# Kernel optimization log

Hardware: AMD Instinct MI355X
Metric: run time of the kernel (lower is better)

Reference implementation:

```python
import jax, jax.numpy as jnp
import numpy as np

NB, NLOC, NALL, NNEI, A_SEL = 1, 512, 640, 96, 20
N_DIM, E_DIM, A_DIM, AXIS = 128, 64, 64, 4
EDGE_INFO = 2 * N_DIM + E_DIM          # 320
SYM = AXIS * (E_DIM + N_DIM)           # 768, cal_1_dim
ANGLE = A_DIM + N_DIM + 2 * E_DIM      # 320, angle_dim


def setup_inputs() -> dict:
    key = jax.random.key(0)
    ks = jax.random.split(key, 16)
    nrm = lambda k, sh, s=1.0: jax.random.normal(k, sh, dtype=jnp.float32) * s

    def lin(k, din, dout, s=0.05):
        k1, k2 = jax.random.split(k)
        return nrm(k1, (din, dout), s), nrm(k2, (dout,), s)

    inp = {}
    inp["g1_ext"] = nrm(ks[0], (NB, NALL, N_DIM))
    inp["g2"] = nrm(ks[1], (NB, NLOC, NNEI, E_DIM))
    inp["h2"] = nrm(ks[2], (NB, NLOC, NNEI, 3))
    inp["angle_embed"] = nrm(ks[3], (NB, NLOC, A_SEL, A_SEL, A_DIM))
    inp["sw"] = jax.random.uniform(ks[4], (NB, NLOC, NNEI), dtype=jnp.float32)
    inp["a_sw"] = jax.random.uniform(ks[5], (NB, NLOC, A_SEL), dtype=jnp.float32)
    inp["w_self"], inp["b_self"] = lin(ks[6], N_DIM, N_DIM)
    inp["w_proj"] = nrm(ks[7], (E_DIM, N_DIM), 0.05)  # proj_g1g2, bias=False
    inp["w_lin1"], inp["b_lin1"] = lin(ks[8], SYM, N_DIM)
    inp["w_edge1"], inp["b_edge1"] = lin(ks[9], EDGE_INFO, N_DIM)
    inp["w_lin2"], inp["b_lin2"] = lin(ks[10], EDGE_INFO, E_DIM)
    inp["w_ang"], inp["b_ang"] = lin(ks[11], ANGLE, A_DIM)
    inp["w_ga1"], inp["b_ga1"] = lin(ks[12], ANGLE, E_DIM)
    inp["w_ga2"], inp["b_ga2"] = lin(ks[13], E_DIM, E_DIM)
    inp["nlist"] = jax.random.randint(ks[14], (NB, NLOC, NNEI), 0, NALL)
    inp["nlist_mask"] = jnp.ones((NB, NLOC, NNEI), dtype=bool)
    inp["a_nlist_mask"] = jnp.ones((NB, NLOC, A_SEL), dtype=bool)
    return inp


def _sym_op(g, h2, mask, sw, axis):
    # symmetrization_op: _cal_hg (smooth, use_sqrt_nnei) followed by _cal_grrg
    # g: nb x nloc x nnei x d, h2: nb x nloc x nnei x 3
    g = jnp.where(mask[..., None], g, 0.0) * sw[..., None]
    inv = np.float32(1.0 / np.sqrt(g.shape[2]))
    hg = jnp.einsum('blnt,blnd->bltd', h2, g) * inv
    grrg = jnp.einsum('bltd,blta->blda', hg, hg[..., :axis])  # nb x nloc x d x axis
    return grrg.reshape(grrg.shape[0], grrg.shape[1], -1)


def reference(g1_ext, g2, h2, angle_embed, sw, a_sw,
              w_self, b_self, w_proj, w_lin1, b_lin1, w_edge1, b_edge1,
              w_lin2, b_lin2, w_ang, b_ang, w_ga1, b_ga1, w_ga2, b_ga2,
              nlist, nlist_mask, a_nlist_mask):
    act = jax.nn.silu
    nb, nloc, nnei, e_dim = g2.shape
    n_dim = g1_ext.shape[-1]
    a_sel = angle_embed.shape[2]
    g1 = g1_ext[:, :nloc]
    # _make_nei_g1: gather neighbor node features, nb x nloc x nnei x n_dim
    gg1 = jnp.take_along_axis(
        g1_ext, nlist.reshape(nb, nloc * nnei, 1), axis=1
    ).reshape(nb, nloc, nnei, n_dim)
    maskf = nlist_mask[..., None]
    swf = sw[..., None]

    g1_update = [g1]
    # node self mlp
    g1_update.append(act(g1 @ w_self + b_self))
    # conv update: masked+switched gg1 times projected g2, mean over nnei
    gg1_ms = jnp.where(maskf, gg1, 0.0) * swf
    g1_update.append(jnp.sum((g2 @ w_proj) * gg1_ms, axis=2) / np.float32(nnei))
    # symmetrized axis-neuron update
    sym = jnp.concatenate(
        [_sym_op(g2, h2, nlist_mask, sw, AXIS),
         _sym_op(gg1, h2, nlist_mask, sw, AXIS)], axis=-1)
    g1_update.append(act(sym @ w_lin1 + b_lin1))
    # edge info: [tiled g1, gg1, g2] -> 2*n_dim + e_dim
    edge_info = jnp.concatenate(
        [jnp.broadcast_to(g1[:, :, None, :], (nb, nloc, nnei, n_dim)), gg1, g2],
        axis=-1)
    g1_edge = act(edge_info @ w_edge1 + b_edge1) * swf
    g1_update.append(jnp.sum(g1_edge, axis=2) / np.float32(nnei))
    # res_avg
    g1_new = sum(g1_update) / np.float32(np.sqrt(len(g1_update)))

    g2_update = [g2, act(edge_info @ w_lin2 + b_lin2)]

    # angle branch: angle_dim = a_dim + n_dim + 2*e_dim
    g2a = jnp.where(a_nlist_mask[..., None], g2[:, :, :a_sel, :], 0.0)
    ang = jnp.concatenate([
        angle_embed,
        jnp.broadcast_to(g1[:, :, None, None, :], (nb, nloc, a_sel, a_sel, n_dim)),
        jnp.broadcast_to(g2a[:, :, :, None, :], (nb, nloc, a_sel, a_sel, e_dim)),
        jnp.broadcast_to(g2a[:, :, None, :, :], (nb, nloc, a_sel, a_sel, e_dim)),
    ], axis=-1)
    a_new = (angle_embed + act(ang @ w_ang + b_ang)) / np.float32(np.sqrt(2.0))

    # angle -> edge message, switch-weighted on both angle axes, mean over one axis
    ang_w = ang * a_sw[:, :, :, None, None] * a_sw[:, :, None, :, None]
    g2_ang = jnp.sum(act(ang_w @ w_ga1 + b_ga1), axis=3) / np.float32(a_sel)
    g2_ang_full = jnp.concatenate(
        [g2_ang, jnp.zeros((nb, nloc, nnei - a_sel, e_dim), g2.dtype)], axis=2)
    g2_update.append(act(g2_ang_full @ w_ga2 + b_ga2))
    g2_new = sum(g2_update) / np.float32(np.sqrt(len(g2_update)))

    return g1_new, g2_new, h2, a_new
```

## Files before the change

kernel.cpp:

```cpp
#include <hip/hip_runtime.h>
#include <hip/hip_bf16.h>

#define NLOC 512
#define NALL 640
#define NNEI 96
#define ASEL 20
#define NDIM 128
#define EDIM 64
#define ADIM 64

typedef short bf16x8 __attribute__((ext_vector_type(8)));
typedef float f32x4 __attribute__((ext_vector_type(4)));
typedef unsigned short ushort8 __attribute__((ext_vector_type(8)));

__device__ __forceinline__ unsigned short f2bf(float f) {
    unsigned int u = __float_as_uint(f);
    unsigned int r = (u + 0x7FFFu + ((u >> 16) & 1u)) >> 16;
    return (unsigned short)r;
}
__device__ __forceinline__ float bf2f(unsigned short u) {
    return __uint_as_float(((unsigned int)u) << 16);
}
__device__ __forceinline__ float silu(float x) { return x / (1.0f + __expf(-x)); }

__device__ __forceinline__ void cvt8_store(unsigned short* dst, const float* src) {
    float4 f0 = *(const float4*)src;
    float4 f1 = *(const float4*)(src + 4);
    ushort8 v;
    v[0] = f2bf(f0.x); v[1] = f2bf(f0.y); v[2] = f2bf(f0.z); v[3] = f2bf(f0.w);
    v[4] = f2bf(f1.x); v[5] = f2bf(f1.y); v[6] = f2bf(f1.z); v[7] = f2bf(f1.w);
    *(ushort8*)dst = v;
}

__global__ void prep_bt2(const float* __restrict__ w_ang, const float* __restrict__ w_ga1,
                         const float* __restrict__ w_edge1, const float* __restrict__ w_lin2,
                         const float* __restrict__ w_proj, const float* __restrict__ w_self,
                         unsigned short* __restrict__ bt_ae, unsigned short* __restrict__ bt_g2e,
                         unsigned short* __restrict__ bt_sm, unsigned short* __restrict__ bt_pij) {
    int idx = blockIdx.x * 256 + threadIdx.x;
    if (idx < 8192) {
        int k = idx & 63, n = idx >> 6;
        bt_ae[idx] = f2bf((n < 64) ? w_ang[k * 64 + n] : w_ga1[k * 64 + (n - 64)]);
    } else if (idx < 32768) {
        int id2 = idx - 8192;
        int k = id2 & 63, n = id2 >> 6;
        float v;
        if (n < 128)      v = w_edge1[(256 + k) * 128 + n];
        else if (n < 192) v = w_lin2[(256 + k) * 64 + (n - 128)];
        else if (n < 256) v = 0.0f;
        else              v = w_proj[k * 128 + (n - 256)];
        bt_g2e[id2] = f2bf(v);
    } else if (idx < 114688) {
        int id3 = idx - 32768;
        int k = id3 & 127, n = id3 >> 7;
        float v;
        if (n < 128)      v = w_edge1[k * 128 + n];
        else if (n < 192) v = w_lin2[k * 64 + (n - 128)];
        else if (n < 320) v = w_edge1[(128 + k) * 128 + (n - 192)];
        else if (n < 384) v = w_lin2[(128 + k) * 64 + (n - 320)];
        else if (n < 512) { int c = n - 384;
            v = (c < 64) ? w_ang[(64 + k) * 64 + c] : w_ga1[(64 + k) * 64 + (c - 64)]; }
        else              v = w_self[k * 128 + (n - 512)];
        bt_sm[id3] = f2bf(v);
    } else {
        int id4 = idx - 114688;
        int k = id4 & 63, n = id4 >> 6;
        float v;
        if (n < 128) v = (n < 64) ? w_ang[(192 + k) * 64 + n] : w_ga1[(192 + k) * 64 + (n - 64)];
        else { int c = n - 128;
            v = (c < 64) ? w_ang[(256 + k) * 64 + c] : w_ga1[(256 + k) * 64 + (c - 64)]; }
        bt_pij[id4] = f2bf(v);
    }
}

__global__ __launch_bounds__(256) void gemm_small(
    const float* __restrict__ g1_ext, const unsigned short* __restrict__ bt_sm,
    const float* __restrict__ b_self, float* __restrict__ P1a, float* __restrict__ g1self,
    float* __restrict__ E1, float* __restrict__ E2) {
    const int m0 = blockIdx.x * 128;
    const int ntile = blockIdx.y;
    __shared__ __align__(16) unsigned short Asl[128 * 136];
    __shared__ __align__(16) unsigned short Bsl[128 * 136];
    const int tid = threadIdx.x;
#pragma unroll
    for (int u = 0; u < 8; u++) {
        int g = tid + u * 256;
        int row = g >> 4, seg = g & 15;
        cvt8_store(&Asl[row * 136 + seg * 8], g1_ext + (m0 + row) * 128 + seg * 8);
        *(ushort8*)&Bsl[row * 136 + seg * 8] =
            *(const ushort8*)&bt_sm[(ntile * 128 + row) * 128 + seg * 8];
    }
    __syncthreads();
    const int lane = tid & 63, wid = tid >> 6;
    const int wr = wid >> 1, wc = wid & 1;
    const int r15 = lane & 15, kg = lane >> 4;
    f32x4 acc[4][4] = {};
#pragma unroll
    for (int h = 0; h < 4; h++) {
        bf16x8 afr[4], bfr[4];
#pragma unroll
        for (int mi = 0; mi < 4; mi++)
            afr[mi] = *(const bf16x8*)&Asl[(wr * 64 + mi * 16 + r15) * 136 + h * 32 + kg * 8];
#pragma unroll
        for (int ni = 0; ni < 4; ni++)
            bfr[ni] = *(const bf16x8*)&Bsl[(wc * 64 + ni * 16 + r15) * 136 + h * 32 + kg * 8];
#pragma unroll
        for (int mi = 0; mi < 4; mi++)
#pragma unroll
            for (int ni = 0; ni < 4; ni++)
                acc[mi][ni] = __builtin_amdgcn_mfma_f32_16x16x32_bf16(afr[mi], bfr[ni], acc[mi][ni], 0, 0, 0);
    }
#pragma unroll
    for (int mi = 0; mi < 4; mi++) {
        int rbase = m0 + wr * 64 + mi * 16 + kg * 4;
#pragma unroll
        for (int ni = 0; ni < 4; ni++) {
            int gc = ntile * 128 + wc * 64 + ni * 16 + r15;
#pragma unroll
            for (int t2 = 0; t2 < 4; t2++) {
                int a = rbase + t2;
                float z = acc[mi][ni][t2];
                if (gc < 192) { if (a < 512) E1[a * 192 + gc] = z; }
                else if (gc < 384) E2[a * 192 + (gc - 192)] = z;
                else if (gc < 512) { if (a < 512) P1a[a * 128 + (gc - 384)] = z; }
                else { if (a < 512) g1self[a * 128 + (gc - 512)] = silu(z + b_self[gc - 512]); }
            }
        }
    }
}

__global__ __launch_bounds__(256) void gemm_pij(
    const float* __restrict__ g2, const unsigned short* __restrict__ bt_pij,
    unsigned short* __restrict__ P_i, unsigned short* __restrict__ P_j) {
    const int m0 = blockIdx.x * 128;
    const int ntile = blockIdx.y;
    __shared__ __align__(16) unsigned short Asl[128 * 72];
    __shared__ __align__(16) unsigned short Bsl[128 * 72];
    const int tid = threadIdx.x;
#pragma unroll
    for (int u = 0; u < 4; u++) {
        int g = tid + u * 256;
        int row = g >> 3, seg = g & 7;
        int li = m0 + row, l = li / 20, i = li - l * 20;
        cvt8_store(&Asl[row * 72 + seg * 8], g2 + (l * 96 + i) * 64 + seg * 8);
        *(ushort8*)&Bsl[row * 72 + seg * 8] =
            *(const ushort8*)&bt_pij[(ntile * 128 + row) * 64 + seg * 8];
    }
    __syncthreads();
    const int lane = tid & 63, wid = tid >> 6;
    const int wr = wid >> 1, wc = wid & 1;
    const int r15 = lane & 15, kg = lane >> 4;
    f32x4 acc[4][4] = {};
#pragma unroll
    for (int h = 0; h < 2; h++) {
        bf16x8 afr[4], bfr[4];
#pragma unroll
        for (int mi = 0; mi < 4; mi++)
            afr[mi] = *(const bf16x8*)&Asl[(wr * 64 + mi * 16 + r15) * 72 + h * 32 + kg * 8];
#pragma unroll
        for (int ni = 0; ni < 4; ni++)
            bfr[ni] = *(const bf16x8*)&Bsl[(wc * 64 + ni * 16 + r15) * 72 + h * 32 + kg * 8];
#pragma unroll
        for (int mi = 0; mi < 4; mi++)
#pragma unroll
            for (int ni = 0; ni < 4; ni++)
                acc[mi][ni] = __builtin_amdgcn_mfma_f32_16x16x32_bf16(afr[mi], bfr[ni], acc[mi][ni], 0, 0, 0);
    }
    unsigned short* Pout = (ntile == 0) ? P_i : P_j;
#pragma unroll
    for (int mi = 0; mi < 4; mi++) {
        int rbase = m0 + wr * 64 + mi * 16 + kg * 4;
#pragma unroll
        for (int ni = 0; ni < 4; ni++) {
            int c = wc * 64 + ni * 16 + r15;
#pragma unroll
            for (int t2 = 0; t2 < 4; t2++)
                Pout[(rbase + t2) * 128 + c] = f2bf(acc[mi][ni][t2]);
        }
    }
}

__global__ void k_sym(const float* __restrict__ g1_ext, const float* __restrict__ g2,
                      const float* __restrict__ h2, const float* __restrict__ sw,
                      const int* __restrict__ nlist, const float* __restrict__ w_lin1,
                      const float* __restrict__ b_lin1, float* __restrict__ term4) {
    int l = blockIdx.x, t = threadIdx.x;
    __shared__ float h2s[96 * 3];
    __shared__ float sws[96];
    __shared__ int nls[96];
    __shared__ float hg[3 * 192];
    __shared__ float symv[768];
    if (t < 96) { sws[t] = sw[l * 96 + t]; nls[t] = nlist[l * 96 + t]; }
    for (int p = t; p < 288; p += 256) h2s[p] = h2[l * 288 + p];
    __syncthreads();
    const float inv = 0.1020620726f;
    for (int p = t; p < 576; p += 256) {
        float acc = 0.0f;
        if (p < 192) {
            int tt = p >> 6, d = p & 63;
            for (int n = 0; n < 96; n++)
                acc += h2s[n * 3 + tt] * g2[(l * 96 + n) * 64 + d] * sws[n];
            hg[tt * 192 + d] = acc * inv;
        } else {
            int q = p - 192;
            int tt = q >> 7, d = q & 127;
            for (int n = 0; n < 96; n++)
                acc += h2s[n * 3 + tt] * g1_ext[nls[n] * 128 + d] * sws[n];
            hg[tt * 192 + 64 + d] = acc * inv;
        }
    }
    __syncthreads();
    for (int p = t; p < 768; p += 256) {
        float acc = 0.0f;
        if (p < 256) {
            int d = p >> 2, a = p & 3;
            for (int tt = 0; tt < 3; tt++) acc += hg[tt * 192 + d] * hg[tt * 192 + a];
        } else {
            int q = p - 256;
            int d = q >> 2, a = q & 3;
            for (int tt = 0; tt < 3; tt++) acc += hg[tt * 192 + 64 + d] * hg[tt * 192 + 64 + a];
        }
        symv[p] = acc;
    }
    __syncthreads();
    if (t < 128) {
        float acc = b_lin1[t];
#pragma unroll 8
        for (int k = 0; k < 768; k++) acc += symv[k] * w_lin1[k * 128 + t];
        term4[l * 128 + t] = silu(acc);
    }
}

__global__ __launch_bounds__(256) void angle_main(
    const float* __restrict__ ae, const unsigned short* __restrict__ bt_ae,
    const float* __restrict__ P1a, const unsigned short* __restrict__ P_i,
    const unsigned short* __restrict__ P_j, const float* __restrict__ a_sw,
    const float* __restrict__ b_ang, const float* __restrict__ b_ga1,
    float* __restrict__ g2acc, float* __restrict__ a_new_out) {
    const int m0 = blockIdx.x * 128;
    __shared__ __align__(16) unsigned short Asl[128 * 72];
    __shared__ __align__(16) unsigned short Bsl[128 * 72];
    const int tid = threadIdx.x;
#pragma unroll
    for (int u = 0; u < 4; u++) {
        int g = tid + u * 256;
        int row = g >> 3, seg = g & 7;
        cvt8_store(&Asl[row * 72 + seg * 8], ae + (m0 + row) * 64 + seg * 8);
        *(ushort8*)&Bsl[row * 72 + seg * 8] = *(const ushort8*)&bt_ae[row * 64 + seg * 8];
    }
    __syncthreads();
    const int lane = tid & 63, wid = tid >> 6;
    const int wr = wid >> 1, wc = wid & 1;
    const int r15 = lane & 15, kg = lane >> 4;
    f32x4 acc[4][4] = {};
#pragma unroll
    for (int h = 0; h < 2; h++) {
        bf16x8 afr[4], bfr[4];
#pragma unroll
        for (int mi = 0; mi < 4; mi++)
            afr[mi] = *(const bf16x8*)&Asl[(wr * 64 + mi * 16 + r15) * 72 + h * 32 + kg * 8];
#pragma unroll
        for (int ni = 0; ni < 4; ni++)
            bfr[ni] = *(const bf16x8*)&Bsl[(wc * 64 + ni * 16 + r15) * 72 + h * 32 + kg * 8];
#pragma unroll
        for (int mi = 0; mi < 4; mi++)
#pragma unroll
            for (int ni = 0; ni < 4; ni++)
                acc[mi][ni] = __builtin_amdgcn_mfma_f32_16x16x32_bf16(afr[mi], bfr[ni], acc[mi][ni], 0, 0, 0);
    }
#pragma unroll
    for (int mi = 0; mi < 4; mi++) {
        int rbase = m0 + wr * 64 + mi * 16 + kg * 4;
        int l = rbase / 400;
        int rem = rbase - l * 400;
        int i = rem / 20;
        int j0 = rem - i * 20;
        const float* p1b = P1a + l * 128;
        const unsigned short* pib = P_i + (l * 20 + i) * 128;
        const unsigned short* pjb = P_j + l * 20 * 128;
#pragma unroll
        for (int ni = 0; ni < 4; ni++) {
            int c = wc * 64 + ni * 16 + r15;
            float base = p1b[c] + bf2f(pib[c]);
            if (c < 64) {
                float bb = b_ang[c];
#pragma unroll
                for (int t2 = 0; t2 < 4; t2++) {
                    int r = rbase + t2, j = j0 + t2;
                    float z = acc[mi][ni][t2] + base + bf2f(pjb[j * 128 + c]);
                    float aev = bf2f(Asl[(rbase - m0 + t2) * 72 + c]);
                    a_new_out[r * 64 + c] = (aev + silu(z + bb)) * 0.70710678f;
                }
            } else {
                int cc = c - 64;
                float bb = b_ga1[cc];
                float swi = a_sw[l * 20 + i];
                float part = 0.0f;
#pragma unroll
                for (int t2 = 0; t2 < 4; t2++) {
                    int j = j0 + t2;
                    float z = acc[mi][ni][t2] + base + bf2f(pjb[j * 128 + c]);
                    float s = swi * a_sw[l * 20 + j];
                    part += silu(s * z + bb);
                }
                atomicAdd(&g2acc[(l * 20 + i) * 64 + cc], part);
            }
        }
    }
}

__global__ void k_f2(const float* __restrict__ g2ang_acc, const float* __restrict__ w_ga2,
                     const float* __restrict__ b_ga2, float* __restrict__ yga2) {
    int l = blockIdx.x, t = threadIdx.x;
    __shared__ float gs[20 * 64];
    for (int p = t; p < 1280; p += 256) gs[p] = g2ang_acc[l * 1280 + p] * 0.05f;
    __syncthreads();
    for (int p = t; p < 1280; p += 256) {
        int i = p >> 6, c = p & 63;
        float acc = b_ga2[c];
#pragma unroll 8
        for (int k = 0; k < 64; k++) acc += gs[i * 64 + k] * w_ga2[k * 64 + c];
        yga2[l * 1280 + p] = silu(acc);
    }
}

__global__ __launch_bounds__(256) void edge_main(
    const float* __restrict__ g1_ext, const float* __restrict__ g2, const float* __restrict__ sw,
    const int* __restrict__ nlist, const unsigned short* __restrict__ bt_g2e,
    const float* __restrict__ E1, const float* __restrict__ E2,
    const float* __restrict__ b_edge1, const float* __restrict__ b_lin2,
    const float* __restrict__ b_ga2, const float* __restrict__ yga2,
    float* __restrict__ g1_acc3, float* __restrict__ g1_acc5, float* __restrict__ g2_new_out) {
    const int m0 = blockIdx.x * 128;
    const int ntile = blockIdx.y;
    __shared__ __align__(16) unsigned short Asl[128 * 72];
    __shared__ __align__(16) unsigned short Bsl[128 * 72];
    const int tid = threadIdx.x;
#pragma unroll
    for (int u = 0; u < 4; u++) {
        int g = tid + u * 256;
        int row = g >> 3, seg = g & 7;
        cvt8_store(&Asl[row * 72 + seg * 8], g2 + (m0 + row) * 64 + seg * 8);
        *(ushort8*)&Bsl[row * 72 + seg * 8] =
            *(const ushort8*)&bt_g2e[(ntile * 128 + row) * 64 + seg * 8];
    }
    __syncthreads();
    const int lane = tid & 63, wid = tid >> 6;
    const int wr = wid >> 1, wc = wid & 1;
    const int r15 = lane & 15, kg = lane >> 4;
    f32x4 acc[4][4] = {};
#pragma unroll
    for (int h = 0; h < 2; h++) {
        bf16x8 afr[4], bfr[4];
#pragma unroll
        for (int mi = 0; mi < 4; mi++)
            afr[mi] = *(const bf16x8*)&Asl[(wr * 64 + mi * 16 + r15) * 72 + h * 32 + kg * 8];
#pragma unroll
        for (int ni = 0; ni < 4; ni++)
            bfr[ni] = *(const bf16x8*)&Bsl[(wc * 64 + ni * 16 + r15) * 72 + h * 32 + kg * 8];
#pragma unroll
        for (int mi = 0; mi < 4; mi++)
#pragma unroll
            for (int ni = 0; ni < 4; ni++)
                acc[mi][ni] = __builtin_amdgcn_mfma_f32_16x16x32_bf16(afr[mi], bfr[ni], acc[mi][ni], 0, 0, 0);
    }
#pragma unroll
    for (int mi = 0; mi < 4; mi++) {
        int rbase = m0 + wr * 64 + mi * 16 + kg * 4;
        int l = rbase / 96;
        int n0 = rbase - l * 96;
#pragma unroll
        for (int ni = 0; ni < 4; ni++) {
            int c = wc * 64 + ni * 16 + r15;
            if (ntile == 0) {
                float e1 = E1[l * 192 + c];
                float bb = b_edge1[c];
                float part = 0.0f;
#pragma unroll
                for (int t2 = 0; t2 < 4; t2++) {
                    int r = rbase + t2;
                    float z = acc[mi][ni][t2] + e1 + E2[nlist[r] * 192 + c];
                    part += silu(z + bb) * sw[r];
                }
                atomicAdd(&g1_acc5[l * 128 + c], part);
            } else if (ntile == 1) {
                if (c < 64) {
                    float e1 = E1[l * 192 + 128 + c];
                    float bb = b_lin2[c];
                    float sb = silu(b_ga2[c]);
#pragma unroll
                    for (int t2 = 0; t2 < 4; t2++) {
                        int r = rbase + t2, n = n0 + t2;
                        float z = acc[mi][ni][t2] + e1 + E2[nlist[r] * 192 + 128 + c];
                        float y = silu(z + bb);
                        float yg = (n < ASEL) ? yga2[(l * 20 + n) * 64 + c] : sb;
                        float g2v = bf2f(Asl[(r - m0) * 72 + c]);
                        g2_new_out[r * 64 + c] = (g2v + y + yg) * 0.57735027f;
                    }
                }
            } else {
                float part = 0.0f;
#pragma unroll
                for (int t2 = 0; t2 < 4; t2++) {
                    int r = rbase + t2;
                    part += acc[mi][ni][t2] * g1_ext[nlist[r] * 128 + c] * sw[r];
                }
                atomicAdd(&g1_acc3[l * 128 + c], part);
            }
        }
    }
}

__global__ void k_f1(const float* __restrict__ g1_ext, const float* __restrict__ g1self,
                     const float* __restrict__ acc3, const float* __restrict__ term4,
                     const float* __restrict__ acc5, float* __restrict__ out_g1) {
    int idx = blockIdx.x * 256 + threadIdx.x;
    float v = g1_ext[idx] + g1self[idx] + acc3[idx] * (1.0f / 96.0f) + term4[idx] +
              acc5[idx] * (1.0f / 96.0f);
    out_g1[idx] = v * 0.4472135955f;
}

extern "C" void kernel_launch(void* const* d_in, const int* in_sizes, int n_in,
                              void* d_out, int out_size, void* d_ws, size_t ws_size,
                              hipStream_t stream) {
    if (n_in < 22 || in_sizes[0] != 81920 || in_sizes[3] != 13107200) return;
    const float* g1_ext = (const float*)d_in[0];
    const float* g2     = (const float*)d_in[1];
    const float* h2     = (const float*)d_in[2];
    const float* ae     = (const float*)d_in[3];
    const float* sw     = (const float*)d_in[4];
    const float* a_sw   = (const float*)d_in[5];
    const float* w_self = (const float*)d_in[6];
    const float* b_self = (const float*)d_in[7];
    const float* w_proj = (const float*)d_in[8];
    const float* w_lin1 = (const float*)d_in[9];
    const float* b_lin1 = (const float*)d_in[10];
    const float* w_edge1= (const float*)d_in[11];
    const float* b_edge1= (const float*)d_in[12];
    const float* w_lin2 = (const float*)d_in[13];
    const float* b_lin2 = (const float*)d_in[14];
    const float* w_ang  = (const float*)d_in[15];
    const float* b_ang  = (const float*)d_in[16];
    const float* w_ga1  = (const float*)d_in[17];
    const float* b_ga1  = (const float*)d_in[18];
    const float* w_ga2  = (const float*)d_in[19];
    const float* b_ga2  = (const float*)d_in[20];
    const int*   nlist  = (const int*)d_in[21];

    float* ws = (float*)d_ws;
    unsigned short* bt_ae  = (unsigned short*)(ws);
    unsigned short* bt_g2e = (unsigned short*)(ws + 4096);
    unsigned short* bt_sm  = (unsigned short*)(ws + 16384);
    unsigned short* bt_pij = (unsigned short*)(ws + 57344);
    float* P1a    = ws + 65536;
    float* E1     = ws + 131072;
    float* E2     = ws + 229376;
    unsigned short* P_i = (unsigned short*)(ws + 352256);
    unsigned short* P_j = (unsigned short*)(ws + 1007616);
    float* g1self = ws + 1662976;
    float* term4  = ws + 1728512;
    float* yga2   = ws + 1794048;
    float* acc3   = ws + 2449408;
    float* acc5   = ws + 2514944;
    float* g2acc  = ws + 2580480;
    if (ws_size < (size_t)3235840 * sizeof(float)) return;

    float* out = (float*)d_out;
    float* out_g1 = out;
    float* out_g2 = out + 65536;
    float* out_h2 = out + 3211264;
    float* out_an = out + 3358720;

    hipMemsetAsync(acc3, 0, (65536 + 65536 + 655360) * sizeof(float), stream);

    prep_bt2<<<512, 256, 0, stream>>>(w_ang, w_ga1, w_edge1, w_lin2, w_proj, w_self,
                                      bt_ae, bt_g2e, bt_sm, bt_pij);
    gemm_small<<<dim3(5, 5), 256, 0, stream>>>(g1_ext, bt_sm, b_self, P1a, g1self, E1, E2);
    gemm_pij<<<dim3(80, 2), 256, 0, stream>>>(g2, bt_pij, P_i, P_j);
    k_sym<<<512, 256, 0, stream>>>(g1_ext, g2, h2, sw, nlist, w_lin1, b_lin1, term4);
    angle_main<<<1600, 256, 0, stream>>>(ae, bt_ae, P1a, P_i, P_j, a_sw, b_ang, b_ga1,
                                         g2acc, out_an);
    k_f2<<<512, 256, 0, stream>>>(g2acc, w_ga2, b_ga2, yga2);
    edge_main<<<dim3(384, 3), 256, 0, stream>>>(g1_ext, g2, sw, nlist, bt_g2e, E1, E2,
                                                b_edge1, b_lin2, b_ga2, yga2,
                                                acc3, acc5, out_g2);
    k_f1<<<256, 256, 0, stream>>>(g1_ext, g1self, acc3, term4, acc5, out_g1);
    hipMemcpyAsync(out_h2, h2, 147456 * sizeof(float), hipMemcpyDeviceToDevice, stream);
}
```

Baseline: 201.9 us.

## Load GEMM weight fragments directly from global, split sym reduction, raise occupancy

Three GEMM kernels stop staging the small bf16 weight tile in shared memory. Each wave now reads its B fragments straight from global memory, where the tile is likely to sit in cache, which halves LDS use per block and removes the staging stores. Launch bounds of 6 blocks per SIMD-group are added to angle_main and edge_main to allow more resident blocks. The final lin1 matvec in k_sym is split across all 256 threads as two K halves combined through shared memory, instead of leaving half the threads idle. The cost is uncoalesced global fragment loads with higher latency, and possible register pressure from the launch bound.

```diff
diff --git a/kernel.cpp b/kernel.cpp
--- a/kernel.cpp
+++ b/kernel.cpp
@@ -135,7 +135,6 @@
     const int m0 = blockIdx.x * 128;
     const int ntile = blockIdx.y;
     __shared__ __align__(16) unsigned short Asl[128 * 72];
-    __shared__ __align__(16) unsigned short Bsl[128 * 72];
     const int tid = threadIdx.x;
 #pragma unroll
     for (int u = 0; u < 4; u++) {
@@ -143,8 +142,6 @@
         int row = g >> 3, seg = g & 7;
         int li = m0 + row, l = li / 20, i = li - l * 20;
         cvt8_store(&Asl[row * 72 + seg * 8], g2 + (l * 96 + i) * 64 + seg * 8);
-        *(ushort8*)&Bsl[row * 72 + seg * 8] =
-            *(const ushort8*)&bt_pij[(ntile * 128 + row) * 64 + seg * 8];
     }
     __syncthreads();
     const int lane = tid & 63, wid = tid >> 6;
@@ -159,7 +156,7 @@
             afr[mi] = *(const bf16x8*)&Asl[(wr * 64 + mi * 16 + r15) * 72 + h * 32 + kg * 8];
 #pragma unroll
         for (int ni = 0; ni < 4; ni++)
-            bfr[ni] = *(const bf16x8*)&Bsl[(wc * 64 + ni * 16 + r15) * 72 + h * 32 + kg * 8];
+            bfr[ni] = *(const bf16x8*)&bt_pij[(ntile * 128 + wc * 64 + ni * 16 + r15) * 64 + h * 32 + kg * 8];
 #pragma unroll
         for (int mi = 0; mi < 4; mi++)
 #pragma unroll
@@ -190,6 +187,7 @@
     __shared__ int nls[96];
     __shared__ float hg[3 * 192];
     __shared__ float symv[768];
+    __shared__ float red[128];
     if (t < 96) { sws[t] = sw[l * 96 + t]; nls[t] = nlist[l * 96 + t]; }
     for (int p = t; p < 288; p += 256) h2s[p] = h2[l * 288 + p];
     __syncthreads();
@@ -223,15 +221,19 @@
         symv[p] = acc;
     }
     __syncthreads();
-    if (t < 128) {
-        float acc = b_lin1[t];
+    {
+        int col = t & 127, half = t >> 7;
+        float acc = 0.0f;
+        int k0 = half * 384;
 #pragma unroll 8
-        for (int k = 0; k < 768; k++) acc += symv[k] * w_lin1[k * 128 + t];
-        term4[l * 128 + t] = silu(acc);
-    }
-}
-
-__global__ __launch_bounds__(256) void angle_main(
+        for (int k = k0; k < k0 + 384; k++) acc += symv[k] * w_lin1[k * 128 + col];
+        if (half) red[col] = acc;
+        __syncthreads();
+        if (!half) term4[l * 128 + col] = silu(acc + red[col] + b_lin1[col]);
+    }
+}
+
+__global__ __launch_bounds__(256, 6) void angle_main(
     const float* __restrict__ ae, const unsigned short* __restrict__ bt_ae,
     const float* __restrict__ P1a, const unsigned short* __restrict__ P_i,
     const unsigned short* __restrict__ P_j, const float* __restrict__ a_sw,
@@ -239,14 +241,12 @@
     float* __restrict__ g2acc, float* __restrict__ a_new_out) {
     const int m0 = blockIdx.x * 128;
     __shared__ __align__(16) unsigned short Asl[128 * 72];
-    __shared__ __align__(16) unsigned short Bsl[128 * 72];
     const int tid = threadIdx.x;
 #pragma unroll
     for (int u = 0; u < 4; u++) {
         int g = tid + u * 256;
         int row = g >> 3, seg = g & 7;
         cvt8_store(&Asl[row * 72 + seg * 8], ae + (m0 + row) * 64 + seg * 8);
-        *(ushort8*)&Bsl[row * 72 + seg * 8] = *(const ushort8*)&bt_ae[row * 64 + seg * 8];
     }
     __syncthreads();
     const int lane = tid & 63, wid = tid >> 6;
@@ -261,7 +261,7 @@
             afr[mi] = *(const bf16x8*)&Asl[(wr * 64 + mi * 16 + r15) * 72 + h * 32 + kg * 8];
 #pragma unroll
         for (int ni = 0; ni < 4; ni++)
-            bfr[ni] = *(const bf16x8*)&Bsl[(wc * 64 + ni * 16 + r15) * 72 + h * 32 + kg * 8];
+            bfr[ni] = *(const bf16x8*)&bt_ae[(wc * 64 + ni * 16 + r15) * 64 + h * 32 + kg * 8];
 #pragma unroll
         for (int mi = 0; mi < 4; mi++)
 #pragma unroll
@@ -324,7 +324,7 @@
     }
 }
 
-__global__ __launch_bounds__(256) void edge_main(
+__global__ __launch_bounds__(256, 6) void edge_main(
     const float* __restrict__ g1_ext, const float* __restrict__ g2, const float* __restrict__ sw,
     const int* __restrict__ nlist, const unsigned short* __restrict__ bt_g2e,
     const float* __restrict__ E1, const float* __restrict__ E2,
@@ -334,15 +334,12 @@
     const int m0 = blockIdx.x * 128;
     const int ntile = blockIdx.y;
     __shared__ __align__(16) unsigned short Asl[128 * 72];
-    __shared__ __align__(16) unsigned short Bsl[128 * 72];
     const int tid = threadIdx.x;
 #pragma unroll
     for (int u = 0; u < 4; u++) {
         int g = tid + u * 256;
         int row = g >> 3, seg = g & 7;
         cvt8_store(&Asl[row * 72 + seg * 8], g2 + (m0 + row) * 64 + seg * 8);
-        *(ushort8*)&Bsl[row * 72 + seg * 8] =
-            *(const ushort8*)&bt_g2e[(ntile * 128 + row) * 64 + seg * 8];
     }
     __syncthreads();
     const int lane = tid & 63, wid = tid >> 6;
@@ -357,7 +354,7 @@
             afr[mi] = *(const bf16x8*)&Asl[(wr * 64 + mi * 16 + r15) * 72 + h * 32 + kg * 8];
 #pragma unroll
         for (int ni = 0; ni < 4; ni++)
-            bfr[ni] = *(const bf16x8*)&Bsl[(wc * 64 + ni * 16 + r15) * 72 + h * 32 + kg * 8];
+            bfr[ni] = *(const bf16x8*)&bt_g2e[(ntile * 128 + wc * 64 + ni * 16 + r15) * 64 + h * 32 + kg * 8];
 #pragma unroll
         for (int mi = 0; mi < 4; mi++)
 #pragma unroll
```

Result: slower. 223.0 us (+10.5%).
